# Optimization experiments

Measured on AMD Instinct MI355X. Metric: run time of the kernel, lower is better.

The kernel has to match this reference:

```python
import jax, jax.numpy as jnp
import numpy as np
import itertools

K = 10            # GFM knn k
SHARP = 20.0      # GMCCE_Sharp
THRESH = 0.5      # GMCCE_Thres


def setup_inputs() -> dict:
    key = jax.random.key(0)
    ks = jax.random.split(key, 5)
    B, D, N = 4, 512, 2048
    return {
        "src_embedding": jax.random.normal(ks[0], (B, D, N), jnp.float32),
        "tgt_embedding": jax.random.normal(ks[1], (B, D, N), jnp.float32),
        "src": jax.random.normal(ks[2], (B, 3, N), jnp.float32),
        "tgt": jax.random.normal(ks[3], (B, 3, N), jnp.float32),
        "temperature": jax.random.uniform(ks[4], (B, 1), jnp.float32) + 0.5,
        "is_corr": 1,
    }


def _knn_tri(x, k, sigma=1.0):
    # x: [B,3,N] -> idx [B,N,k] of largest gaussian weights (nearest points)
    pts = x.transpose(0, 2, 1)                      # [B,N,3]
    sq = jnp.sum(pts * pts, -1)                     # [B,N]
    d2 = sq[:, :, None] + sq[:, None, :] - 2.0 * jnp.einsum('bnd,bmd->bnm', pts, pts)
    d2 = jnp.maximum(d2, 0.0)
    w = jnp.exp(-d2 / (2.0 * sigma ** 2))
    _, idx = jax.lax.top_k(w, k)
    return idx


def _get_tri(pcd, tri_idx):
    # pcd: [B,N,3], tri_idx: [B,N,P,3] point indices -> [B,N,P,3] sorted (0,0,area)
    B = pcd.shape[0]
    b = jnp.arange(B)[:, None, None, None]
    pts = pcd[b, tri_idx]                           # [B,N,P,3pts,3xyz]
    e1 = pts[..., 1, :] - pts[..., 0, :]
    e2 = pts[..., 2, :] - pts[..., 0, :]
    normals = jnp.cross(e1, e2)
    areas = 0.5 * jnp.linalg.norm(normals, axis=-1)  # [B,N,P]
    z = jnp.zeros_like(areas)
    return jnp.sort(jnp.stack([areas, z, z], -1), axis=-1)


def _gfm(src, tgt, Sharp, Threshold, k=10, eps=1e-6):
    # src: [B,3,N]; tgt: [B,N,3] (corr points)
    B, _, N = src.shape
    idx = _knn_tri(src, k)                                            # [B,N,k]
    pairs = np.asarray(list(itertools.combinations(range(k), 2)))     # [P,2], P=45
    idx_pairs = idx[:, :, pairs]                                      # [B,N,P,2]
    index = jnp.broadcast_to(jnp.arange(N)[None, :, None, None], (B, N, pairs.shape[0], 1))
    tri_idx = jnp.concatenate([index, idx_pairs], -1)                 # [B,N,P,3]
    ls = _get_tri(src.transpose(0, 2, 1), tri_idx)
    lt = _get_tri(tgt, tri_idx) + eps
    loss = jnp.sum((ls - lt) ** 2, -1) / jnp.sum((ls + lt) ** 2, -1)  # [B,N,P]
    loss = jnp.sort(loss, -1)
    reg = jnp.linalg.norm(ls - lt, axis=-1)                           # unsorted, as in torch
    loss = loss + 0.1 * reg
    med = jnp.median(loss, axis=-1, keepdims=True)
    loss = jnp.where(loss > 3.0 * med, 0.0, loss)
    loss = jnp.mean(jnp.sqrt(loss[:, :, :k] + eps), -1)               # [B,N]
    loss = loss - jnp.min(loss, -1, keepdims=True)
    w = 2.0 * jax.nn.sigmoid(-Sharp * loss)
    return jnp.where(w > Threshold, 1.0, 0.0)


def _procrustes(X, Y, w, eps=1e-7):
    # X,Y: [N,3]; w: [N]
    W1 = jnp.sum(jnp.abs(w))
    wn = jnp.broadcast_to(w[:, None], X.shape) / (W1 + eps)
    mux = jnp.sum(wn * X, 0, keepdims=True)
    muy = jnp.sum(wn * Y, 0, keepdims=True)
    Sxy = (Y - muy).T @ (wn * (X - mux))
    U, _, Vh = jnp.linalg.svd(Sxy)
    det = jnp.linalg.det(U) * jnp.linalg.det(Vh)
    d = jnp.where(det < 0.0, jnp.array([1.0, 1.0, -1.0]), jnp.array([1.0, 1.0, 1.0]))
    R = (U * d[None, :]) @ Vh
    t = muy[0] - R @ mux[0]
    return R, t


def reference(src_embedding, tgt_embedding, src, tgt, temperature, is_corr):
    B, _, N = src.shape
    d_k = src_embedding.shape[1]
    scores = jnp.einsum('bdn,bdm->bnm', src_embedding, tgt_embedding) / jnp.sqrt(jnp.float32(d_k))
    scores = jax.nn.softmax(10000.0 * scores, axis=-1)
    corres = jnp.argmax(scores, -1)                                   # [B,N]
    corr_tgt = jnp.einsum('bnm,bmd->bnd', scores, tgt.transpose(0, 2, 1))
    weight = _gfm(src, corr_tgt, SHARP, THRESH, K)                    # [B,N]
    src_t = src.transpose(0, 2, 1)
    tgt_t = tgt.transpose(0, 2, 1)
    src_corr = jnp.take_along_axis(tgt_t, corres[..., None], axis=1)  # [B,N,3]
    w_d = jax.lax.stop_gradient(weight)                               # torch detaches weight
    R, T = jax.vmap(_procrustes)(src_t, src_corr, w_d)
    return R, T, corres[..., None], weight[..., None]
```

## Files before the change

### kernel.cpp

```cpp
#include <hip/hip_runtime.h>
#include <math.h>

#define NPTS 2048
#define DIM  512
#define BATCH 4
#define KNN 10
#define NPAIR 45
#define MSPLIT 32
#define CSPLIT 8
#define CCHUNK (NPTS / CSPLIT)
#define KB (DIM / 16)

typedef _Float16 half8  __attribute__((ext_vector_type(8)));
typedef float    f32x16 __attribute__((ext_vector_type(16)));

__device__ __forceinline__ void gload_lds16(const _Float16* g, _Float16* l)
{
    __builtin_amdgcn_global_load_lds(
        (const __attribute__((address_space(1))) void*)g,
        (__attribute__((address_space(3))) void*)l, 16, 0, 0);
}

__global__ __launch_bounds__(256) void transpose_split(
    const float* __restrict__ srcEmb, const float* __restrict__ tgtEmb,
    _Float16* __restrict__ srcT_hi, _Float16* __restrict__ srcT_lo,
    _Float16* __restrict__ tgtT_hi, _Float16* __restrict__ tgtT_lo)
{
    __shared__ float ldsT[32][65];
    int blk = blockIdx.x;
    const int nt    = blk & 31;
    const int dt    = (blk >> 5) & 15;
    const int b     = (blk >> 9) & 3;
    const int which = blk >> 11;
    const float* in = (which == 0 ? srcEmb : tgtEmb) + (size_t)b * DIM * NPTS;
    _Float16* outHi = (which == 0 ? srcT_hi : tgtT_hi) + (size_t)b * NPTS * DIM;
    _Float16* outLo = (which == 0 ? srcT_lo : tgtT_lo) + (size_t)b * NPTS * DIM;
    const int tid = threadIdx.x;
#pragma unroll
    for (int i = 0; i < 2; ++i) {
        int id = tid + i * 256;
        int r = id >> 4, c4 = id & 15;
        float4 v = *(const float4*)(in + (size_t)(dt * 32 + r) * NPTS + nt * 64 + c4 * 4);
        ldsT[r][c4 * 4 + 0] = v.x; ldsT[r][c4 * 4 + 1] = v.y;
        ldsT[r][c4 * 4 + 2] = v.z; ldsT[r][c4 * 4 + 3] = v.w;
    }
    __syncthreads();
    const int nrow = tid >> 2, dseg = (tid & 3) * 8;
    __align__(16) _Float16 hb[8];
    __align__(16) _Float16 lb[8];
#pragma unroll
    for (int j = 0; j < 8; ++j) {
        float a = ldsT[dseg + j][nrow];
        _Float16 h = (_Float16)a;
        float r = a - (float)h;
        hb[j] = h;
        lb[j] = (_Float16)(r * 2048.0f);
    }
    const int n  = nt * 64 + nrow;
    const int d0 = dt * 32 + dseg;
    size_t off = ((size_t)(n >> 5) * KB + (d0 >> 4)) * 512
               + (size_t)((d0 >> 3) & 1) * 256 + (size_t)(n & 31) * 8;
    *(half8*)(outHi + off) = *(half8*)hb;
    *(half8*)(outLo + off) = *(half8*)lb;
}

__global__ __launch_bounds__(256, 2) void gemm_argmax(
    const _Float16* __restrict__ Ahi, const _Float16* __restrict__ Alo,
    const _Float16* __restrict__ Bhi, const _Float16* __restrict__ Blo,
    float* __restrict__ partV, int* __restrict__ partI)
{
    __shared__ _Float16 smem[2][32 * 512];
    const int tid  = threadIdx.x;
    int blk = blockIdx.x;
    const int nt = blk & 15, mt = (blk >> 4) & 15, b = blk >> 8;
    const int lane = tid & 63, wave = tid >> 6;
    const int wm = (wave & 1) * 64, wn = (wave >> 1) * 64;

    const _Float16* baseArr =
        (wave == 0) ? Ahi : (wave == 1) ? Alo : (wave == 2) ? Bhi : Blo;
    const int rt = (wave < 2) ? mt : nt;
    const _Float16* gbase = baseArr + (size_t)b * NPTS * DIM
                          + (size_t)(rt * 4) * KB * 512 + (size_t)lane * 8;
    const int ldsW = wave * 8 * 512;
    const int laneoff = lane * 8;

    f32x16 accH[2][2], accX[2][2];
#pragma unroll
    for (int mi = 0; mi < 2; ++mi)
#pragma unroll
        for (int ni = 0; ni < 2; ++ni)
#pragma unroll
            for (int r = 0; r < 16; ++r) { accH[mi][ni][r] = 0.f; accX[mi][ni][r] = 0.f; }

#pragma unroll
    for (int i = 0; i < 8; ++i)
        gload_lds16(gbase + ((size_t)(i >> 1) * KB + (i & 1)) * 512,
                    &smem[0][ldsW + i * 512]);
    __syncthreads();

    int cur = 0;
    for (int t = 0; t < 16; ++t) {
        if (t < 15) {
#pragma unroll
            for (int i = 0; i < 8; ++i)
                gload_lds16(gbase + ((size_t)(i >> 1) * KB + (2 * (t + 1) + (i & 1))) * 512,
                            &smem[cur ^ 1][ldsW + i * 512]);
        }
        const _Float16* sb = &smem[cur][0];
#pragma unroll
        for (int ks = 0; ks < 2; ++ks) {
            half8 aF[2][2], bF[2][2];
#pragma unroll
            for (int mi = 0; mi < 2; ++mi)
#pragma unroll
                for (int h = 0; h < 2; ++h)
                    aF[mi][h] = *(const half8*)&sb[(h * 8 + ((wave & 1) * 2 + mi) * 2 + ks) * 512 + laneoff];
#pragma unroll
            for (int ni = 0; ni < 2; ++ni)
#pragma unroll
                for (int h = 0; h < 2; ++h)
                    bF[ni][h] = *(const half8*)&sb[((2 + h) * 8 + ((wave >> 1) * 2 + ni) * 2 + ks) * 512 + laneoff];
#pragma unroll
            for (int mi = 0; mi < 2; ++mi)
#pragma unroll
                for (int ni = 0; ni < 2; ++ni) {
                    accH[mi][ni] = __builtin_amdgcn_mfma_f32_32x32x16_f16(aF[mi][0], bF[ni][0], accH[mi][ni], 0, 0, 0);
                    accX[mi][ni] = __builtin_amdgcn_mfma_f32_32x32x16_f16(aF[mi][0], bF[ni][1], accX[mi][ni], 0, 0, 0);
                    accX[mi][ni] = __builtin_amdgcn_mfma_f32_32x32x16_f16(aF[mi][1], bF[ni][0], accX[mi][ni], 0, 0, 0);
                }
        }
        __syncthreads();
        cur ^= 1;
    }

    const float inv2048 = 1.0f / 2048.0f;
#pragma unroll
    for (int ni = 0; ni < 2; ++ni) {
        float bv = -INFINITY; int bi = 0x7fffffff;
#pragma unroll
        for (int mi = 0; mi < 2; ++mi)
#pragma unroll
            for (int r = 0; r < 16; ++r) {
                float v = accH[mi][ni][r] + accX[mi][ni][r] * inv2048;
                int m = mt * 128 + wm + mi * 32 + (r & 3) + 8 * (r >> 2) + 4 * (lane >> 5);
                if (v > bv || (v == bv && m < bi)) { bv = v; bi = m; }
            }
        float ov = __shfl_xor(bv, 32);
        int   oi = __shfl_xor(bi, 32);
        if (ov > bv || (ov == bv && oi < bi)) { bv = ov; bi = oi; }
        if (lane < 32) {
            int n = nt * 128 + wn + ni * 32 + lane;
            int s = mt * 2 + (wm >> 6);
            partV[((size_t)b * NPTS + n) * MSPLIT + s] = bv;
            partI[((size_t)b * NPTS + n) * MSPLIT + s] = bi;
        }
    }
}

__global__ void argmax_combine(const float* __restrict__ partV,
                               const int* __restrict__ partI,
                               int* __restrict__ corres,
                               float* __restrict__ outCorres)
{
    const int g = blockIdx.x * 256 + threadIdx.x;
    if (g >= BATCH * NPTS) return;
    float bv = -INFINITY; int bi = 0x7fffffff;
    for (int s = 0; s < MSPLIT; ++s) {
        float v = partV[(size_t)g * MSPLIT + s];
        int  ii = partI[(size_t)g * MSPLIT + s];
        if (v > bv || (v == bv && ii < bi)) { bv = v; bi = ii; }
    }
    corres[g] = bi;
    outCorres[g] = (float)bi;
}

__global__ __launch_bounds__(256, 8) void knn_part(
    const float* __restrict__ src,
    unsigned int* __restrict__ partK, int* __restrict__ partI)
{
    __shared__ float4 cpts[CCHUNK];
    __shared__ unsigned int   candK[CSPLIT][32][KNN];
    __shared__ unsigned short candI[CSPLIT][32][KNN];

    int blk = blockIdx.x;
    const int cs = blk & 7;  blk >>= 3;
    const int qg = blk & 63; blk >>= 6;
    const int b  = blk;
    const int tid = threadIdx.x;
    const float* S = src + (size_t)b * 3 * NPTS;

    {
        const int m = cs * CCHUNK + tid;
        float qx = S[m], qy = S[NPTS + m], qz = S[2 * NPTS + m];
        float qq = __fadd_rn(__fadd_rn(__fmul_rn(qx, qx), __fmul_rn(qy, qy)), __fmul_rn(qz, qz));
        cpts[tid] = make_float4(qx, qy, qz, qq);
    }
    __syncthreads();

    const int nl = tid & 31;
    const int sl = tid >> 5;
    const int n  = qg * 32 + nl;
    const float px = S[n], py = S[NPTS + n], pz = S[2 * NPTS + n];
    const float psq = __fadd_rn(__fadd_rn(__fmul_rn(px, px), __fmul_rn(py, py)), __fmul_rn(pz, pz));

    unsigned int bk[KNN]; int bi[KNN];
#pragma unroll
    for (int j = 0; j < KNN; ++j) { bk[j] = 0u; bi[j] = 0; }

    const int t0 = sl * 32;
    for (int j = 0; j < 32; ++j) {
        const int t = t0 + j;
        float4 c = cpts[t];
        float dot = __fadd_rn(__fadd_rn(__fmul_rn(px, c.x), __fmul_rn(py, c.y)), __fmul_rn(pz, c.z));
        float d2  = __fsub_rn(__fadd_rn(psq, c.w), __fmul_rn(2.f, dot));
        d2 = fmaxf(d2, 0.f);
        float w = expf(-0.5f * d2);
        unsigned int k = __float_as_uint(w);
        if (k > bk[KNN - 1]) {
            unsigned int ck = k; int ci = cs * CCHUNK + t;
#pragma unroll
            for (int q = 0; q < KNN; ++q) {
                bool gt = ck > bk[q];
                unsigned int tk = bk[q]; int ti = bi[q];
                bk[q] = gt ? ck : tk;  bi[q] = gt ? ci : ti;
                ck    = gt ? tk : ck;  ci    = gt ? ti : ci;
            }
        }
    }
#pragma unroll
    for (int j = 0; j < KNN; ++j) {
        candK[sl][nl][j] = bk[j];
        candI[sl][nl][j] = (unsigned short)bi[j];
    }
    __syncthreads();

    if (tid < 32) {
        int cur[CSPLIT] = {0, 0, 0, 0, 0, 0, 0, 0};
        const size_t base = (((size_t)b * NPTS + qg * 32 + tid) * CSPLIT + cs) * KNN;
        for (int sel = 0; sel < KNN; ++sel) {
            unsigned int bw = 0u; int bi2 = 0x7fffffff; int bs = -1;
#pragma unroll
            for (int s = 0; s < CSPLIT; ++s) {
                if (cur[s] < KNN) {
                    unsigned int k2 = candK[s][tid][cur[s]];
                    int i2 = (int)candI[s][tid][cur[s]];
                    if (k2 > bw || (k2 == bw && i2 < bi2)) { bw = k2; bi2 = i2; bs = s; }
                }
            }
            partK[base + sel] = bw;
            partI[base + sel] = bi2;
#pragma unroll
            for (int s = 0; s < CSPLIT; ++s) if (s == bs) cur[s]++;
        }
    }
}

__global__ void knn_merge(const unsigned int* __restrict__ partK,
                          const int* __restrict__ partI,
                          int* __restrict__ knnIdx)
{
    const int g = blockIdx.x * 256 + threadIdx.x;
    if (g >= BATCH * NPTS) return;
    const size_t base = (size_t)g * CSPLIT * KNN;
    int cur[CSPLIT] = {0, 0, 0, 0, 0, 0, 0, 0};
    for (int sel = 0; sel < KNN; ++sel) {
        unsigned int bw = 0u; int bi = 0x7fffffff; int bs = -1;
#pragma unroll
        for (int s = 0; s < CSPLIT; ++s) {
            if (cur[s] < KNN) {
                unsigned int k2 = partK[base + s * KNN + cur[s]];
                int i2 = partI[base + s * KNN + cur[s]];
                if (k2 > bw || (k2 == bw && i2 < bi)) { bw = k2; bi = i2; bs = s; }
            }
        }
        knnIdx[(size_t)g * KNN + sel] = bi;
#pragma unroll
        for (int s = 0; s < CSPLIT; ++s) if (s == bs) cur[s]++;
    }
}

__device__ const int PAIR_A[NPAIR] = {
    0,0,0,0,0,0,0,0,0, 1,1,1,1,1,1,1,1, 2,2,2,2,2,2,2,
    3,3,3,3,3,3, 4,4,4,4,4, 5,5,5,5, 6,6,6, 7,7, 8};
__device__ const int PAIR_C[NPAIR] = {
    1,2,3,4,5,6,7,8,9, 2,3,4,5,6,7,8,9, 3,4,5,6,7,8,9,
    4,5,6,7,8,9, 5,6,7,8,9, 6,7,8,9, 7,8,9, 8,9, 9};

__global__ __launch_bounds__(256) void loss_kernel(
    const float* __restrict__ src, const float* __restrict__ tgt,
    const int* __restrict__ corres, const int* __restrict__ knn,
    float* __restrict__ lossOut)
{
    const int wave = threadIdx.x >> 6;
    const int lane = threadIdx.x & 63;
    const int g = blockIdx.x * 4 + wave;
    const int b = g >> 11;
    const int n = g & (NPTS - 1);
    const float* S = src + (size_t)b * 3 * NPTS;
    const float* T = tgt + (size_t)b * 3 * NPTS;
    const int* cor = corres + b * NPTS;

    const float eps = 1e-6f;
    const float e2 = __fmul_rn(eps, eps);
    const float two_e2 = __fadd_rn(e2, e2);

    float Lv = INFINITY, Rv = 0.f;
    if (lane < NPAIR) {
        const int a = PAIR_A[lane], c = PAIR_C[lane];
        const int ia = knn[(size_t)g * KNN + a];
        const int ic = knn[(size_t)g * KNN + c];
        const float P0x = S[n], P0y = S[NPTS + n], P0z = S[2 * NPTS + n];
        const int c0 = cor[n];
        const float Q0x = T[c0], Q0y = T[NPTS + c0], Q0z = T[2 * NPTS + c0];

        float e1x = S[ia] - P0x, e1y = S[NPTS + ia] - P0y, e1z = S[2 * NPTS + ia] - P0z;
        float g2x = S[ic] - P0x, g2y = S[NPTS + ic] - P0y, g2z = S[2 * NPTS + ic] - P0z;
        float nx = __fsub_rn(__fmul_rn(e1y, g2z), __fmul_rn(e1z, g2y));
        float ny = __fsub_rn(__fmul_rn(e1z, g2x), __fmul_rn(e1x, g2z));
        float nz = __fsub_rn(__fmul_rn(e1x, g2y), __fmul_rn(e1y, g2x));
        float as_ = 0.5f * sqrtf(__fadd_rn(__fadd_rn(__fmul_rn(nx, nx), __fmul_rn(ny, ny)), __fmul_rn(nz, nz)));

        const int ca = cor[ia], cc = cor[ic];
        float f1x = T[ca] - Q0x, f1y = T[NPTS + ca] - Q0y, f1z = T[2 * NPTS + ca] - Q0z;
        float h2x = T[cc] - Q0x, h2y = T[NPTS + cc] - Q0y, h2z = T[2 * NPTS + cc] - Q0z;
        float mx = __fsub_rn(__fmul_rn(f1y, h2z), __fmul_rn(f1z, h2y));
        float my = __fsub_rn(__fmul_rn(f1z, h2x), __fmul_rn(f1x, h2z));
        float mz = __fsub_rn(__fmul_rn(f1x, h2y), __fmul_rn(f1y, h2x));
        float at_ = 0.5f * sqrtf(__fadd_rn(__fadd_rn(__fmul_rn(mx, mx), __fmul_rn(my, my)), __fmul_rn(mz, mz)));

        float lt3 = __fadd_rn(at_, eps);
        float d  = __fsub_rn(as_, lt3);
        float s  = __fadd_rn(as_, lt3);
        float num = __fadd_rn(two_e2, __fmul_rn(d, d));
        float den = __fadd_rn(two_e2, __fmul_rn(s, s));
        Lv = num / den;
        Rv = sqrtf(num);
    }

    float sl = Lv;
#pragma unroll
    for (int k = 2; k <= 64; k <<= 1)
#pragma unroll
        for (int j = k >> 1; j > 0; j >>= 1) {
            float other = __shfl_xor(sl, j);
            bool up = ((lane & k) == 0);
            bool lower = ((lane & j) == 0);
            sl = (up == lower) ? fminf(sl, other) : fmaxf(sl, other);
        }

    float comb = __fadd_rn(sl, __fmul_rn(0.1f, Rv));
    if (lane >= NPAIR) comb = INFINITY;

    float cs = comb;
#pragma unroll
    for (int k = 2; k <= 64; k <<= 1)
#pragma unroll
        for (int j = k >> 1; j > 0; j >>= 1) {
            float other = __shfl_xor(cs, j);
            bool up = ((lane & k) == 0);
            bool lower = ((lane & j) == 0);
            cs = (up == lower) ? fminf(cs, other) : fmaxf(cs, other);
        }
    float med = __shfl(cs, 22);
    float thr = __fmul_rn(3.0f, med);

    float v = 0.f;
    if (lane < KNN) {
        float x = comb;
        if (x > thr) x = 0.f;
        v = sqrtf(__fadd_rn(x, eps));
    }
#pragma unroll
    for (int j = 32; j > 0; j >>= 1) v += __shfl_xor(v, j);
    if (lane == 0) lossOut[g] = v / 10.0f;
}

__global__ void min_kernel(const float* __restrict__ loss, float* __restrict__ minOut)
{
    __shared__ float red[256];
    const int b = blockIdx.x;
    float m = INFINITY;
    for (int n = threadIdx.x; n < NPTS; n += 256) m = fminf(m, loss[b * NPTS + n]);
    red[threadIdx.x] = m; __syncthreads();
    for (int s = 128; s > 0; s >>= 1) {
        if (threadIdx.x < s) red[threadIdx.x] = fminf(red[threadIdx.x], red[threadIdx.x + s]);
        __syncthreads();
    }
    if (threadIdx.x == 0) minOut[b] = red[0];
}

__global__ void weight_kernel(const float* __restrict__ loss, const float* __restrict__ minv,
                              float* __restrict__ wOut, float* __restrict__ wWs)
{
    const int g = blockIdx.x * 256 + threadIdx.x;
    if (g >= BATCH * NPTS) return;
    const int b = g >> 11;
    float l = __fsub_rn(loss[g], minv[b]);
    float el = expf(20.0f * l);
    float sg = 1.0f / (1.0f + el);
    float w = 2.0f * sg;
    float res = (w > 0.5f) ? 1.0f : 0.0f;
    wOut[g] = res;
    wWs[g] = res;
}

__device__ inline double det3(const double M[3][3])
{
    return M[0][0] * (M[1][1] * M[2][2] - M[1][2] * M[2][1])
         - M[0][1] * (M[1][0] * M[2][2] - M[1][2] * M[2][0])
         + M[0][2] * (M[1][0] * M[2][1] - M[1][1] * M[2][0]);
}

__global__ __launch_bounds__(256) void procrustes_kernel(
    const float* __restrict__ src, const float* __restrict__ tgt,
    const int* __restrict__ corres, const float* __restrict__ weight,
    float* __restrict__ outRT)
{
    __shared__ double red[256];
    __shared__ double sh[16];
    const int b = blockIdx.x;
    const int tid = threadIdx.x;
    const float* S = src + (size_t)b * 3 * NPTS;
    const float* T = tgt + (size_t)b * 3 * NPTS;
    const int* cor = corres + b * NPTS;
    const float* w = weight + b * NPTS;

    double a7[7] = {0, 0, 0, 0, 0, 0, 0};
    for (int n = tid; n < NPTS; n += 256) {
        double wn = w[n];
        if (wn != 0.0) {
            double x0 = S[n], x1 = S[NPTS + n], x2 = S[2 * NPTS + n];
            int c = cor[n];
            double y0 = T[c], y1 = T[NPTS + c], y2 = T[2 * NPTS + c];
            a7[0] += wn;
            a7[1] += wn * x0; a7[2] += wn * x1; a7[3] += wn * x2;
            a7[4] += wn * y0; a7[5] += wn * y1; a7[6] += wn * y2;
        }
    }
    for (int q = 0; q < 7; ++q) {
        red[tid] = a7[q]; __syncthreads();
        for (int s2 = 128; s2 > 0; s2 >>= 1) {
            if (tid < s2) red[tid] += red[tid + s2];
            __syncthreads();
        }
        if (tid == 0) sh[q] = red[0];
        __syncthreads();
    }
    const double W1 = sh[0];
    const double denom = W1 + 1e-7;
    const double mux0 = sh[1] / denom, mux1 = sh[2] / denom, mux2 = sh[3] / denom;
    const double muy0 = sh[4] / denom, muy1 = sh[5] / denom, muy2 = sh[6] / denom;

    double a9[9] = {0, 0, 0, 0, 0, 0, 0, 0, 0};
    for (int n = tid; n < NPTS; n += 256) {
        double wn = w[n];
        if (wn != 0.0) {
            double ww = wn / denom;
            double x0 = ww * ((double)S[n] - mux0);
            double x1 = ww * ((double)S[NPTS + n] - mux1);
            double x2 = ww * ((double)S[2 * NPTS + n] - mux2);
            int c = cor[n];
            double y0 = (double)T[c] - muy0;
            double y1 = (double)T[NPTS + c] - muy1;
            double y2 = (double)T[2 * NPTS + c] - muy2;
            a9[0] += y0 * x0; a9[1] += y0 * x1; a9[2] += y0 * x2;
            a9[3] += y1 * x0; a9[4] += y1 * x1; a9[5] += y1 * x2;
            a9[6] += y2 * x0; a9[7] += y2 * x1; a9[8] += y2 * x2;
        }
    }
    for (int q = 0; q < 9; ++q) {
        red[tid] = a9[q]; __syncthreads();
        for (int s2 = 128; s2 > 0; s2 >>= 1) {
            if (tid < s2) red[tid] += red[tid + s2];
            __syncthreads();
        }
        if (tid == 0) sh[q] = red[0];
        __syncthreads();
    }

    if (tid == 0) {
        double Ae[3][3] = {{sh[0], sh[1], sh[2]}, {sh[3], sh[4], sh[5]}, {sh[6], sh[7], sh[8]}};
        double M[3][3], V[3][3] = {{1, 0, 0}, {0, 1, 0}, {0, 0, 1}};
        for (int i = 0; i < 3; ++i)
            for (int j = 0; j < 3; ++j) {
                double s2 = 0;
                for (int k = 0; k < 3; ++k) s2 += Ae[k][i] * Ae[k][j];
                M[i][j] = s2;
            }
        const int pp[3] = {0, 0, 1}, qq[3] = {1, 2, 2};
        for (int sweep = 0; sweep < 60; ++sweep) {
            double off = fabs(M[0][1]) + fabs(M[0][2]) + fabs(M[1][2]);
            if (off < 1e-30) break;
            for (int e = 0; e < 3; ++e) {
                int p = pp[e], q = qq[e];
                double apq = M[p][q];
                if (fabs(apq) < 1e-300) continue;
                double app = M[p][p], aqq = M[q][q];
                double theta = (aqq - app) / (2.0 * apq);
                double t = ((theta >= 0) ? 1.0 : -1.0) / (fabs(theta) + sqrt(theta * theta + 1.0));
                double cc = 1.0 / sqrt(t * t + 1.0), ss = t * cc;
                int r = 3 - p - q;
                double mrp = M[r][p], mrq = M[r][q];
                M[p][p] = app - t * apq;
                M[q][q] = aqq + t * apq;
                M[p][q] = M[q][p] = 0.0;
                M[r][p] = M[p][r] = cc * mrp - ss * mrq;
                M[r][q] = M[q][r] = ss * mrp + cc * mrq;
                for (int k = 0; k < 3; ++k) {
                    double vp = V[k][p], vq = V[k][q];
                    V[k][p] = cc * vp - ss * vq;
                    V[k][q] = ss * vp + cc * vq;
                }
            }
        }
        double ev[3] = {M[0][0], M[1][1], M[2][2]};
        int o[3] = {0, 1, 2};
        for (int i = 0; i < 2; ++i)
            for (int j = 0; j < 2 - i; ++j)
                if (ev[o[j]] < ev[o[j + 1]]) { int tswap = o[j]; o[j] = o[j + 1]; o[j + 1] = tswap; }
        double Vs[3][3], Us[3][3], sig[3];
        for (int k = 0; k < 3; ++k) {
            sig[k] = sqrt(fmax(ev[o[k]], 0.0));
            for (int i = 0; i < 3; ++i) Vs[i][k] = V[i][o[k]];
        }
        for (int k = 0; k < 3; ++k) {
            double u0 = Ae[0][0] * Vs[0][k] + Ae[0][1] * Vs[1][k] + Ae[0][2] * Vs[2][k];
            double u1 = Ae[1][0] * Vs[0][k] + Ae[1][1] * Vs[1][k] + Ae[1][2] * Vs[2][k];
            double u2 = Ae[2][0] * Vs[0][k] + Ae[2][1] * Vs[1][k] + Ae[2][2] * Vs[2][k];
            if (sig[k] > 1e-12 * sig[0] + 1e-300) {
                Us[0][k] = u0 / sig[k]; Us[1][k] = u1 / sig[k]; Us[2][k] = u2 / sig[k];
            } else if (k == 2) {
                double cx = Us[1][0] * Us[2][1] - Us[2][0] * Us[1][1];
                double cy = Us[2][0] * Us[0][1] - Us[0][0] * Us[2][1];
                double cz = Us[0][0] * Us[1][1] - Us[1][0] * Us[0][1];
                double nn = sqrt(cx * cx + cy * cy + cz * cz);
                if (nn < 1e-300) { cx = 0; cy = 0; cz = 1; nn = 1; }
                Us[0][2] = cx / nn; Us[1][2] = cy / nn; Us[2][2] = cz / nn;
            } else {
                Us[0][k] = (k == 0) ? 1 : 0; Us[1][k] = (k == 1) ? 1 : 0; Us[2][k] = 0;
            }
        }
        double detU = det3(Us), detV = det3(Vs);
        double dsg = (detU * detV < 0.0) ? -1.0 : 1.0;
        double R[3][3];
        for (int i = 0; i < 3; ++i)
            for (int j = 0; j < 3; ++j) {
                R[i][j] = Us[i][0] * Vs[j][0] + Us[i][1] * Vs[j][1] + dsg * Us[i][2] * Vs[j][2];
                outRT[b * 9 + i * 3 + j] = (float)R[i][j];
            }
        double mu_x[3] = {mux0, mux1, mux2};
        double mu_y[3] = {muy0, muy1, muy2};
        for (int i = 0; i < 3; ++i) {
            double ti = mu_y[i] - (R[i][0] * mu_x[0] + R[i][1] * mu_x[1] + R[i][2] * mu_x[2]);
            outRT[36 + b * 3 + i] = (float)ti;
        }
    }
}

extern "C" void kernel_launch(void* const* d_in, const int* in_sizes, int n_in,
                              void* d_out, int out_size, void* d_ws, size_t ws_size,
                              hipStream_t stream)
{
    const float* srcEmb = (const float*)d_in[0];
    const float* tgtEmb = (const float*)d_in[1];
    const float* src    = (const float*)d_in[2];
    const float* tgt    = (const float*)d_in[3];
    float* out = (float*)d_out;

    char* wsp = (char*)d_ws;
    const size_t TSZ = (size_t)BATCH * NPTS * DIM * sizeof(_Float16);
    _Float16* tgtT_hi = (_Float16*)wsp;                 wsp += TSZ;
    _Float16* tgtT_lo = (_Float16*)wsp;                 wsp += TSZ;
    _Float16* srcT_hi = (_Float16*)wsp;                 wsp += TSZ;
    _Float16* srcT_lo = (_Float16*)wsp;                 wsp += TSZ;
    float* wsPartV = (float*)wsp;                       wsp += (size_t)BATCH * NPTS * MSPLIT * 4;
    int*   wsPartI = (int*)wsp;                         wsp += (size_t)BATCH * NPTS * MSPLIT * 4;
    int*   wsCorres = (int*)wsp;                        wsp += BATCH * NPTS * 4;
    int*   wsKnn    = (int*)wsp;                        wsp += BATCH * NPTS * KNN * 4;
    float* wsLoss   = (float*)wsp;                      wsp += BATCH * NPTS * 4;
    float* wsMin    = (float*)wsp;                      wsp += 256;
    float* wsWeight = (float*)wsp;                      wsp += BATCH * NPTS * 4;

    unsigned int* knnPartK = (unsigned int*)tgtT_hi;
    int*          knnPartI = (int*)tgtT_lo;

    float* outCorres = out + 48;
    float* outWeight = out + 48 + BATCH * NPTS;

    transpose_split<<<dim3(4096), dim3(256), 0, stream>>>(
        srcEmb, tgtEmb, srcT_hi, srcT_lo, tgtT_hi, tgtT_lo);
    gemm_argmax<<<dim3(1024), dim3(256), 0, stream>>>(
        tgtT_hi, tgtT_lo, srcT_hi, srcT_lo, wsPartV, wsPartI);
    argmax_combine<<<dim3((BATCH * NPTS + 255) / 256), dim3(256), 0, stream>>>(
        wsPartV, wsPartI, wsCorres, outCorres);
    knn_part<<<dim3(BATCH * 64 * CSPLIT), dim3(256), 0, stream>>>(src, knnPartK, knnPartI);
    knn_merge<<<dim3((BATCH * NPTS + 255) / 256), dim3(256), 0, stream>>>(
        knnPartK, knnPartI, wsKnn);
    loss_kernel<<<dim3(BATCH * NPTS / 4), dim3(256), 0, stream>>>(
        src, tgt, wsCorres, wsKnn, wsLoss);
    min_kernel<<<dim3(BATCH), dim3(256), 0, stream>>>(wsLoss, wsMin);
    weight_kernel<<<dim3((BATCH * NPTS + 255) / 256), dim3(256), 0, stream>>>(
        wsLoss, wsMin, outWeight, wsWeight);
    procrustes_kernel<<<dim3(BATCH), dim3(256), 0, stream>>>(
        src, tgt, wsCorres, wsWeight, out);
}
```

Baseline: 180.6 us.

## Use fp16 hi-only GEMM with top-2 margin check and exact repair of near-ties

Drops the hi/lo split-precision correction in the score GEMM so that each tile issues one MFMA instead of three and stages half as much data in LDS. Each partial argmax now also tracks the runner-up value. Rows whose top-two margin falls below a fixed tolerance are added to a list, and a repair kernel recomputes those rows at hi+lo precision. The block order is also swizzled and occupancy is raised to 3 blocks per CU. The cost is an extra partial-value buffer, an atomic flag list, a memset and an added kernel launch. Correctness now depends on the tolerance covering the fp16 error, and flagged rows beyond the 1024 cap are silently left unrepaired.

```diff
diff --git a/kernel.cpp b/kernel.cpp
--- a/kernel.cpp
+++ b/kernel.cpp
@@ -10,6 +10,8 @@
 #define CSPLIT 8
 #define CCHUNK (NPTS / CSPLIT)
 #define KB (DIM / 16)
+#define TAU 0.15f
+#define MAXFLAG 1024
 
 typedef _Float16 half8  __attribute__((ext_vector_type(8)));
 typedef float    f32x16 __attribute__((ext_vector_type(16)));
@@ -64,114 +66,183 @@
     *(half8*)(outLo + off) = *(half8*)lb;
 }
 
-__global__ __launch_bounds__(256, 2) void gemm_argmax(
-    const _Float16* __restrict__ Ahi, const _Float16* __restrict__ Alo,
-    const _Float16* __restrict__ Bhi, const _Float16* __restrict__ Blo,
-    float* __restrict__ partV, int* __restrict__ partI)
-{
-    __shared__ _Float16 smem[2][32 * 512];
-    const int tid  = threadIdx.x;
-    int blk = blockIdx.x;
+__global__ __launch_bounds__(256, 3) void gemm_hh(
+    const _Float16* __restrict__ Ahi,
+    const _Float16* __restrict__ Bhi,
+    float* __restrict__ partV, int* __restrict__ partI, float* __restrict__ partV2)
+{
+    __shared__ _Float16 smem[2][16 * 512];
+    const int tid = threadIdx.x;
+    const int p = blockIdx.x;
+    const int blk = (p & 7) * 128 + (p >> 3);
     const int nt = blk & 15, mt = (blk >> 4) & 15, b = blk >> 8;
     const int lane = tid & 63, wave = tid >> 6;
     const int wm = (wave & 1) * 64, wn = (wave >> 1) * 64;
 
-    const _Float16* baseArr =
-        (wave == 0) ? Ahi : (wave == 1) ? Alo : (wave == 2) ? Bhi : Blo;
-    const int rt = (wave < 2) ? mt : nt;
-    const _Float16* gbase = baseArr + (size_t)b * NPTS * DIM
-                          + (size_t)(rt * 4) * KB * 512 + (size_t)lane * 8;
-    const int ldsW = wave * 8 * 512;
+    const _Float16* pbase[4];
+#pragma unroll
+    for (int i = 0; i < 4; ++i) {
+        const int f = wave * 4 + i;
+        const int isB = f >> 3;
+        const int rb = (f >> 1) & 3, kb2 = f & 1;
+        const _Float16* arr = isB ? Bhi : Ahi;
+        const int rt = isB ? nt : mt;
+        pbase[i] = arr + (size_t)b * NPTS * DIM
+                 + ((size_t)(rt * 4 + rb) * KB + kb2) * 512 + (size_t)lane * 8;
+    }
     const int laneoff = lane * 8;
 
-    f32x16 accH[2][2], accX[2][2];
+    f32x16 acc[2][2];
 #pragma unroll
     for (int mi = 0; mi < 2; ++mi)
 #pragma unroll
         for (int ni = 0; ni < 2; ++ni)
 #pragma unroll
-            for (int r = 0; r < 16; ++r) { accH[mi][ni][r] = 0.f; accX[mi][ni][r] = 0.f; }
-
-#pragma unroll
-    for (int i = 0; i < 8; ++i)
-        gload_lds16(gbase + ((size_t)(i >> 1) * KB + (i & 1)) * 512,
-                    &smem[0][ldsW + i * 512]);
+            for (int r = 0; r < 16; ++r) acc[mi][ni][r] = 0.f;
+
+#pragma unroll
+    for (int i = 0; i < 4; ++i)
+        gload_lds16(pbase[i], &smem[0][(wave * 4 + i) * 512]);
     __syncthreads();
 
     int cur = 0;
     for (int t = 0; t < 16; ++t) {
         if (t < 15) {
 #pragma unroll
-            for (int i = 0; i < 8; ++i)
-                gload_lds16(gbase + ((size_t)(i >> 1) * KB + (2 * (t + 1) + (i & 1))) * 512,
-                            &smem[cur ^ 1][ldsW + i * 512]);
+            for (int i = 0; i < 4; ++i)
+                gload_lds16(pbase[i] + (size_t)(t + 1) * 1024,
+                            &smem[cur ^ 1][(wave * 4 + i) * 512]);
         }
         const _Float16* sb = &smem[cur][0];
 #pragma unroll
         for (int ks = 0; ks < 2; ++ks) {
-            half8 aF[2][2], bF[2][2];
+            half8 aF[2], bF[2];
 #pragma unroll
             for (int mi = 0; mi < 2; ++mi)
-#pragma unroll
-                for (int h = 0; h < 2; ++h)
-                    aF[mi][h] = *(const half8*)&sb[(h * 8 + ((wave & 1) * 2 + mi) * 2 + ks) * 512 + laneoff];
+                aF[mi] = *(const half8*)&sb[(((wave & 1) * 2 + mi) * 2 + ks) * 512 + laneoff];
 #pragma unroll
             for (int ni = 0; ni < 2; ++ni)
-#pragma unroll
-                for (int h = 0; h < 2; ++h)
-                    bF[ni][h] = *(const half8*)&sb[((2 + h) * 8 + ((wave >> 1) * 2 + ni) * 2 + ks) * 512 + laneoff];
+                bF[ni] = *(const half8*)&sb[(8 + ((wave >> 1) * 2 + ni) * 2 + ks) * 512 + laneoff];
 #pragma unroll
             for (int mi = 0; mi < 2; ++mi)
 #pragma unroll
-                for (int ni = 0; ni < 2; ++ni) {
-                    accH[mi][ni] = __builtin_amdgcn_mfma_f32_32x32x16_f16(aF[mi][0], bF[ni][0], accH[mi][ni], 0, 0, 0);
-                    accX[mi][ni] = __builtin_amdgcn_mfma_f32_32x32x16_f16(aF[mi][0], bF[ni][1], accX[mi][ni], 0, 0, 0);
-                    accX[mi][ni] = __builtin_amdgcn_mfma_f32_32x32x16_f16(aF[mi][1], bF[ni][0], accX[mi][ni], 0, 0, 0);
-                }
+                for (int ni = 0; ni < 2; ++ni)
+                    acc[mi][ni] = __builtin_amdgcn_mfma_f32_32x32x16_f16(aF[mi], bF[ni], acc[mi][ni], 0, 0, 0);
         }
         __syncthreads();
         cur ^= 1;
     }
 
-    const float inv2048 = 1.0f / 2048.0f;
 #pragma unroll
     for (int ni = 0; ni < 2; ++ni) {
-        float bv = -INFINITY; int bi = 0x7fffffff;
+        float b1 = -INFINITY; int i1 = 0x7fffffff; float b2 = -INFINITY;
 #pragma unroll
         for (int mi = 0; mi < 2; ++mi)
 #pragma unroll
             for (int r = 0; r < 16; ++r) {
-                float v = accH[mi][ni][r] + accX[mi][ni][r] * inv2048;
+                float v = acc[mi][ni][r];
                 int m = mt * 128 + wm + mi * 32 + (r & 3) + 8 * (r >> 2) + 4 * (lane >> 5);
-                if (v > bv || (v == bv && m < bi)) { bv = v; bi = m; }
-            }
-        float ov = __shfl_xor(bv, 32);
-        int   oi = __shfl_xor(bi, 32);
-        if (ov > bv || (ov == bv && oi < bi)) { bv = ov; bi = oi; }
+                if (v > b1) { b2 = b1; b1 = v; i1 = m; }
+                else if (v > b2) b2 = v;
+            }
+        float o1 = __shfl_xor(b1, 32);
+        int   oi = __shfl_xor(i1, 32);
+        float o2 = __shfl_xor(b2, 32);
+        if (o1 > b1 || (o1 == b1 && oi < i1)) { b2 = fmaxf(b1, o2); b1 = o1; i1 = oi; }
+        else b2 = fmaxf(b2, o1);
         if (lane < 32) {
             int n = nt * 128 + wn + ni * 32 + lane;
             int s = mt * 2 + (wm >> 6);
-            partV[((size_t)b * NPTS + n) * MSPLIT + s] = bv;
-            partI[((size_t)b * NPTS + n) * MSPLIT + s] = bi;
-        }
-    }
-}
-
-__global__ void argmax_combine(const float* __restrict__ partV,
-                               const int* __restrict__ partI,
-                               int* __restrict__ corres,
-                               float* __restrict__ outCorres)
+            size_t q = ((size_t)b * NPTS + n) * MSPLIT + s;
+            partV[q] = b1; partI[q] = i1; partV2[q] = b2;
+        }
+    }
+}
+
+__global__ void argmax_combine_hh(
+    const float* __restrict__ partV, const int* __restrict__ partI,
+    const float* __restrict__ partV2,
+    int* __restrict__ corres, float* __restrict__ outCorres,
+    int* __restrict__ flagCnt, int* __restrict__ flagList)
 {
     const int g = blockIdx.x * 256 + threadIdx.x;
     if (g >= BATCH * NPTS) return;
-    float bv = -INFINITY; int bi = 0x7fffffff;
+    float v1 = -INFINITY; int i1 = 0x7fffffff;
+    float v2 = -INFINITY;
+    float w2 = -INFINITY;
     for (int s = 0; s < MSPLIT; ++s) {
-        float v = partV[(size_t)g * MSPLIT + s];
-        int  ii = partI[(size_t)g * MSPLIT + s];
-        if (v > bv || (v == bv && ii < bi)) { bv = v; bi = ii; }
-    }
-    corres[g] = bi;
-    outCorres[g] = (float)bi;
+        float V  = partV[(size_t)g * MSPLIT + s];
+        int   I  = partI[(size_t)g * MSPLIT + s];
+        float V2 = partV2[(size_t)g * MSPLIT + s];
+        if (V > v1) { v2 = fmaxf(v2, v1); v1 = V; i1 = I; w2 = V2; }
+        else        { v2 = fmaxf(v2, V); }
+    }
+    corres[g] = i1;
+    outCorres[g] = (float)i1;
+    float second = fmaxf(v2, w2);
+    if (v1 - second < TAU) {
+        int pos = atomicAdd(flagCnt, 1);
+        if (pos < MAXFLAG) flagList[pos] = g;
+    }
+}
+
+__global__ __launch_bounds__(256) void repair_kernel(
+    const _Float16* __restrict__ tgtT_hi, const _Float16* __restrict__ tgtT_lo,
+    const _Float16* __restrict__ srcT_hi, const _Float16* __restrict__ srcT_lo,
+    const int* __restrict__ flagCnt, const int* __restrict__ flagList,
+    int* __restrict__ corres, float* __restrict__ outCorres)
+{
+    __shared__ float sA[DIM];
+    __shared__ float rv[256];
+    __shared__ int   ri[256];
+    const float invs = 1.0f / 2048.0f;
+    int cnt = *flagCnt; if (cnt > MAXFLAG) cnt = MAXFLAG;
+    const int tid = threadIdx.x;
+    for (int j = blockIdx.x; j < cnt; j += gridDim.x) {
+        const int g = flagList[j];
+        const int b = g >> 11, n = g & (NPTS - 1);
+        for (int k = tid; k < DIM; k += 256) {
+            size_t off = (size_t)b * NPTS * DIM
+                       + ((size_t)(n >> 5) * KB + (k >> 4)) * 512
+                       + (size_t)((k >> 3) & 1) * 256 + (size_t)(n & 31) * 8 + (k & 7);
+            sA[k] = (float)srcT_hi[off] + (float)srcT_lo[off] * invs;
+        }
+        __syncthreads();
+        float best = -INFINITY; int bi = 0x7fffffff;
+        for (int q = 0; q < 8; ++q) {
+            const int m = q * 256 + tid;
+            const size_t rowb = (size_t)b * NPTS * DIM
+                              + (size_t)(m >> 5) * KB * 512 + (size_t)(m & 31) * 8;
+            float dot = 0.f;
+            for (int kb = 0; kb < KB; ++kb) {
+#pragma unroll
+                for (int hh = 0; hh < 2; ++hh) {
+                    size_t off = rowb + (size_t)kb * 512 + hh * 256;
+                    half8 th = *(const half8*)(tgtT_hi + off);
+                    half8 tl = *(const half8*)(tgtT_lo + off);
+#pragma unroll
+                    for (int e = 0; e < 8; ++e) {
+                        float tb = (float)th[e] + (float)tl[e] * invs;
+                        dot = fmaf(tb, sA[kb * 16 + hh * 8 + e], dot);
+                    }
+                }
+            }
+            if (dot > best) { best = dot; bi = m; }
+        }
+        rv[tid] = best; ri[tid] = bi;
+        __syncthreads();
+        for (int s = 128; s > 0; s >>= 1) {
+            if (tid < s) {
+                if (rv[tid + s] > rv[tid] ||
+                    (rv[tid + s] == rv[tid] && ri[tid + s] < ri[tid])) {
+                    rv[tid] = rv[tid + s]; ri[tid] = ri[tid + s];
+                }
+            }
+            __syncthreads();
+        }
+        if (tid == 0) { corres[g] = ri[0]; outCorres[g] = (float)ri[0]; }
+        __syncthreads();
+    }
 }
 
 __global__ __launch_bounds__(256, 8) void knn_part(
@@ -573,13 +644,16 @@
     _Float16* tgtT_lo = (_Float16*)wsp;                 wsp += TSZ;
     _Float16* srcT_hi = (_Float16*)wsp;                 wsp += TSZ;
     _Float16* srcT_lo = (_Float16*)wsp;                 wsp += TSZ;
-    float* wsPartV = (float*)wsp;                       wsp += (size_t)BATCH * NPTS * MSPLIT * 4;
-    int*   wsPartI = (int*)wsp;                         wsp += (size_t)BATCH * NPTS * MSPLIT * 4;
+    float* wsPartV  = (float*)wsp;                      wsp += (size_t)BATCH * NPTS * MSPLIT * 4;
+    int*   wsPartI  = (int*)wsp;                        wsp += (size_t)BATCH * NPTS * MSPLIT * 4;
+    float* wsPartV2 = (float*)wsp;                      wsp += (size_t)BATCH * NPTS * MSPLIT * 4;
     int*   wsCorres = (int*)wsp;                        wsp += BATCH * NPTS * 4;
     int*   wsKnn    = (int*)wsp;                        wsp += BATCH * NPTS * KNN * 4;
     float* wsLoss   = (float*)wsp;                      wsp += BATCH * NPTS * 4;
     float* wsMin    = (float*)wsp;                      wsp += 256;
     float* wsWeight = (float*)wsp;                      wsp += BATCH * NPTS * 4;
+    int*   wsFlagCnt  = (int*)wsp;                      wsp += 64;
+    int*   wsFlagList = (int*)wsp;                      wsp += MAXFLAG * 4;
 
     unsigned int* knnPartK = (unsigned int*)tgtT_hi;
     int*          knnPartI = (int*)tgtT_lo;
@@ -587,12 +661,16 @@
     float* outCorres = out + 48;
     float* outWeight = out + 48 + BATCH * NPTS;
 
+    hipMemsetAsync(wsFlagCnt, 0, sizeof(int), stream);
+
     transpose_split<<<dim3(4096), dim3(256), 0, stream>>>(
         srcEmb, tgtEmb, srcT_hi, srcT_lo, tgtT_hi, tgtT_lo);
-    gemm_argmax<<<dim3(1024), dim3(256), 0, stream>>>(
-        tgtT_hi, tgtT_lo, srcT_hi, srcT_lo, wsPartV, wsPartI);
-    argmax_combine<<<dim3((BATCH * NPTS + 255) / 256), dim3(256), 0, stream>>>(
-        wsPartV, wsPartI, wsCorres, outCorres);
+    gemm_hh<<<dim3(1024), dim3(256), 0, stream>>>(
+        tgtT_hi, srcT_hi, wsPartV, wsPartI, wsPartV2);
+    argmax_combine_hh<<<dim3((BATCH * NPTS + 255) / 256), dim3(256), 0, stream>>>(
+        wsPartV, wsPartI, wsPartV2, wsCorres, outCorres, wsFlagCnt, wsFlagList);
+    repair_kernel<<<dim3(256), dim3(256), 0, stream>>>(
+        tgtT_hi, tgtT_lo, srcT_hi, srcT_lo, wsFlagCnt, wsFlagList, wsCorres, outCorres);
     knn_part<<<dim3(BATCH * 64 * CSPLIT), dim3(256), 0, stream>>>(src, knnPartK, knnPartI);
     knn_merge<<<dim3((BATCH * NPTS + 255) / 256), dim3(256), 0, stream>>>(
         knnPartK, knnPartI, wsKnn);
```

Measured after the change: 245.3 us. +35.9%, slower.
